# Kernel tuning notes

Measured on AMD Instinct MI355X. Metric: run time of the kernel, lower is better.

## Reference

```python
import jax, jax.numpy as jnp
import numpy as np

H = W = 2048
TANH_C = 1.1486328125  # probability-correction constant from the model
DEG2RAD = np.float32(np.pi / 180.0)

# Fire-spread direction angle (degrees, East=0, counterclockwise) from the
# neighbor at 3x3 window position (r, c) toward the center cell.
DIR_DEG = jnp.array([[315., 270., 225.],
                     [  0.,   0., 180.],
                     [ 45.,  90., 135.]], dtype=jnp.float32)
CENTER_MASK = jnp.ones((3, 3), jnp.float32).at[1, 1].set(0.0)  # exclude self


def _neighborhood(x):
    """x: [H,W] -> [H,W,3,3] with [i,j,r,c] = x[i+r-1, j+c-1], zero padded."""
    xp = jnp.pad(x, 1)
    return jnp.stack(
        [jnp.stack([xp[r:r + H, c:c + W] for c in range(3)], axis=-1)
         for r in range(3)], axis=-2)


def setup_inputs() -> dict:
    key = jax.random.key(0)
    ks = jax.random.split(key, 8)
    p_veg = jax.random.uniform(ks[0], (H, W), jnp.float32)
    p_den = jax.random.uniform(ks[1], (H, W), jnp.float32)
    wind_velocity = jax.random.uniform(ks[2], (H, W), jnp.float32) * 10.0
    wind_towards_direction = jax.random.uniform(ks[3], (H, W), jnp.float32) * 360.0
    slope = (jax.random.uniform(ks[4], (H, W, 3, 3), jnp.float32) - 0.5) * 60.0
    burning = jax.random.uniform(ks[5], (H, W)) < 0.01  # sparse initial ignition
    burned = jnp.zeros((H, W), dtype=bool)
    rand_ignite = jax.random.uniform(ks[6], (H, W), jnp.float32)
    rand_continue = jax.random.uniform(ks[7], (H, W), jnp.float32)
    return dict(
        p_veg=p_veg, p_den=p_den,
        wind_velocity=wind_velocity, wind_towards_direction=wind_towards_direction,
        slope=slope,
        a=jnp.float32(0.1), p_h=jnp.float32(0.3),
        c_1=jnp.float32(0.1), c_2=jnp.float32(0.1), p_continue=jnp.float32(0.3),
        rand_ignite=rand_ignite, rand_continue=rand_continue,
        burning=burning, burned=burned,
    )


def reference(p_veg, p_den, wind_velocity, wind_towards_direction, slope,
              a, p_h, c_1, c_2, p_continue,
              rand_ignite, rand_continue, burning, burned):
    # p_w = exp(c1*V) * exp(c2*V*(cos(theta_w)-1)), theta_w = angle between
    # wind direction and per-neighbor spread direction. [H,W,3,3]
    theta_w = (wind_towards_direction[..., None, None] - DIR_DEG) * DEG2RAD
    p_w = (jnp.exp(c_1 * wind_velocity)[..., None, None]
           * jnp.exp(c_2 * wind_velocity[..., None, None] * (jnp.cos(theta_w) - 1.0)))
    # p_s = exp(a * theta_s), slope angle in radians. [H,W,3,3]
    p_s = jnp.exp(a * slope * DEG2RAD)
    # p_propagate = tanh(c * p_h*(1+p_veg)*(1+p_den)*p_w*p_s)
    p_base = p_h * (1.0 + p_veg) * (1.0 + p_den)  # [H,W]
    p_prop = jnp.tanh(TANH_C * (p_base[..., None, None] * p_w * p_s))
    # 8-neighbor burning indicators (center masked out). [H,W,3,3]
    nbr_burning = _neighborhood(burning.astype(jnp.float32)) * CENTER_MASK
    # p_ignite = 1 - prod_j (1 - p_propagate_j * burning_j)
    p_ignite = 1.0 - jnp.prod(1.0 - p_prop * nbr_burning, axis=(-2, -1))
    # Stochastic state transition.
    burnable = ~burning & ~burned
    new_ignited = burnable & (rand_ignite < p_ignite)
    keep = burning & (rand_continue < p_continue)
    new_burning = new_ignited | keep
    new_burned = burned | (burning & ~keep)
    return p_ignite, jnp.stack([new_burning, new_burned])
```

## Files before the change

### kernel.cpp

```cpp
#include <hip/hip_runtime.h>
#include <math.h>

namespace {

constexpr int H = 2048;
constexpr int W = 2048;
constexpr float TANH_C  = 1.1486328125f;
constexpr float DEG2RAD = 0.017453292519943295f;

__global__ __launch_bounds__(256) void wildfire_step(
    const float* __restrict__ p_veg,  const float* __restrict__ p_den,
    const float* __restrict__ wind_v, const float* __restrict__ wind_d,
    const float* __restrict__ slope,
    const float* __restrict__ s_a,  const float* __restrict__ s_ph,
    const float* __restrict__ s_c1, const float* __restrict__ s_c2,
    const float* __restrict__ s_pc,
    const float* __restrict__ rand_ig, const float* __restrict__ rand_co,
    const int* __restrict__ burning, const int* __restrict__ burned,
    float* __restrict__ out)
{
    __shared__ float sb[3][260];
    const int t  = (int)threadIdx.x;
    const int i  = (int)blockIdx.y;
    const int j0 = (int)blockIdx.x * 256;
    const int j  = j0 + t;

    for (int r = 0; r < 3; ++r) {
        const int ii = i + r - 1;
        for (int c = t; c < 258; c += 256) {
            const int jj = j0 - 1 + c;
            float v = 0.f;
            if (ii >= 0 && ii < H && jj >= 0 && jj < W)
                v = burning[ii * W + jj] ? 1.f : 0.f;
            sb[r][c] = v;
        }
    }
    __syncthreads();

    const float b0 = sb[0][t], b1 = sb[0][t+1], b2 = sb[0][t+2];
    const float b3 = sb[1][t], bc = sb[1][t+1], b5 = sb[1][t+2];
    const float b6 = sb[2][t], b7 = sb[2][t+1], b8 = sb[2][t+2];

    const int   idx       = i * W + j;
    const bool  is_burning = (bc != 0.f);
    const int   was_burned = burned[idx];
    const float rco        = rand_co[idx];
    const float p_cont     = s_pc[0];

    const float any_n = b0 + b1 + b2 + b3 + b5 + b6 + b7 + b8;

    float p_ignite   = 0.f;
    bool  new_ignited = false;

    if (__any(any_n != 0.f)) {
        const float a   = s_a[0];
        const float p_h = s_ph[0];
        const float c1  = s_c1[0];
        const float c2  = s_c2[0];
        const float pv  = p_veg[idx];
        const float pd  = p_den[idx];
        const float wv  = wind_v[idx];
        const float wd  = wind_d[idx];

        const float ew     = expf(c1 * wv);
        const float cvw    = c2 * wv;
        const float p_base = (p_h * (1.f + pv)) * (1.f + pd);
        const float* sl    = slope + (size_t)idx * 9;

        float prod = 1.f;
#define NEIGHBOR(bk, dirdeg, si)                                           \
        if (__any(bk != 0.f)) {                                            \
            const float ct = cosf((wd - dirdeg) * DEG2RAD);                \
            const float pw = ew * expf(cvw * (ct - 1.f));                  \
            const float ps = expf((a * sl[si]) * DEG2RAD);                 \
            const float pp = tanhf(TANH_C * ((p_base * pw) * ps));         \
            prod *= 1.f - pp * bk;                                         \
        }
        NEIGHBOR(b0, 315.f, 0)
        NEIGHBOR(b1, 270.f, 1)
        NEIGHBOR(b2, 225.f, 2)
        NEIGHBOR(b3,   0.f, 3)
        NEIGHBOR(b5, 180.f, 5)
        NEIGHBOR(b6,  45.f, 6)
        NEIGHBOR(b7,  90.f, 7)
        NEIGHBOR(b8, 135.f, 8)
#undef NEIGHBOR
        p_ignite = 1.f - prod;

        const float rig = rand_ig[idx];
        new_ignited = (!is_burning) && (was_burned == 0) && (rig < p_ignite);
    }

    const bool keep = is_burning && (rco < p_cont);
    const bool nb   = new_ignited || keep;
    const bool nd   = (was_burned != 0) || (is_burning && !keep);

    out[idx]             = p_ignite;
    out[H * W + idx]     = nb ? 1.f : 0.f;
    out[2 * H * W + idx] = nd ? 1.f : 0.f;
}

}

extern "C" void kernel_launch(void* const* d_in, const int* in_sizes, int n_in,
                              void* d_out, int out_size, void* d_ws, size_t ws_size,
                              hipStream_t stream)
{
    (void)in_sizes; (void)n_in; (void)out_size; (void)d_ws; (void)ws_size;
    dim3 grid(W / 256, H, 1);
    dim3 block(256, 1, 1);
    hipLaunchKernelGGL(wildfire_step, grid, block, 0, stream,
        (const float*)d_in[0],  (const float*)d_in[1],
        (const float*)d_in[2],  (const float*)d_in[3],
        (const float*)d_in[4],
        (const float*)d_in[5],  (const float*)d_in[6],
        (const float*)d_in[7],  (const float*)d_in[8],
        (const float*)d_in[9],
        (const float*)d_in[10], (const float*)d_in[11],
        (const int*)d_in[12],   (const int*)d_in[13],
        (float*)d_out);
}
```

Measured before the change: 341.2 us.

## Replace per-neighbor trig and tanh with angle-addition and single-division product

Computes cos and sin of the wind angle once and derives each neighbor's cosine by the angle-addition identity with constant direction components. Each neighbor's two exps are folded into one exp(u) scaled by a precomputed factor. The term 1 - tanh(z) is rewritten as 2/(exp(2z)+1), so the product over neighbors becomes one division of accumulated numerators by denominators. All eight neighbors are now computed without per-neighbor wave-uniform branches, and all loads are issued up front. This cuts transcendental work and divergent branching but computes the unused neighbors too, and exp(2z) can overflow to inf for large z (that case still gives p_ignite near 1).

```diff
diff --git a/kernel.cpp b/kernel.cpp
--- a/kernel.cpp
+++ b/kernel.cpp
@@ -7,6 +7,7 @@
 constexpr int W = 2048;
 constexpr float TANH_C  = 1.1486328125f;
 constexpr float DEG2RAD = 0.017453292519943295f;
+constexpr float RT2H    = 0.70710678118654752f;
 
 __global__ __launch_bounds__(256) void wildfire_step(
     const float* __restrict__ p_veg,  const float* __restrict__ p_den,
@@ -41,7 +42,7 @@
     const float b3 = sb[1][t], bc = sb[1][t+1], b5 = sb[1][t+2];
     const float b6 = sb[2][t], b7 = sb[2][t+1], b8 = sb[2][t+2];
 
-    const int   idx       = i * W + j;
+    const int   idx        = i * W + j;
     const bool  is_burning = (bc != 0.f);
     const int   was_burned = burned[idx];
     const float rco        = rand_co[idx];
@@ -49,45 +50,53 @@
 
     const float any_n = b0 + b1 + b2 + b3 + b5 + b6 + b7 + b8;
 
-    float p_ignite   = 0.f;
+    float p_ignite    = 0.f;
     bool  new_ignited = false;
 
     if (__any(any_n != 0.f)) {
+        const float pv  = p_veg[idx];
+        const float pd  = p_den[idx];
+        const float wv  = wind_v[idx];
+        const float wd  = wind_d[idx];
+        const float rig = rand_ig[idx];
+        float sl[9];
+        __builtin_memcpy(sl, slope + (size_t)idx * 9, 9 * sizeof(float));
+
         const float a   = s_a[0];
         const float p_h = s_ph[0];
         const float c1  = s_c1[0];
         const float c2  = s_c2[0];
-        const float pv  = p_veg[idx];
-        const float pd  = p_den[idx];
-        const float wv  = wind_v[idx];
-        const float wd  = wind_d[idx];
 
-        const float ew     = expf(c1 * wv);
-        const float cvw    = c2 * wv;
+        const float wr  = wd * DEG2RAD;
+        const float cw  = cosf(wr);
+        const float sw  = sinf(wr);
+        const float ew  = expf(c1 * wv);
+        const float cvw = c2 * wv;
+        const float asl = a * DEG2RAD;
         const float p_base = (p_h * (1.f + pv)) * (1.f + pd);
-        const float* sl    = slope + (size_t)idx * 9;
+        const float Cz  = TANH_C * (p_base * ew);
 
-        float prod = 1.f;
-#define NEIGHBOR(bk, dirdeg, si)                                           \
-        if (__any(bk != 0.f)) {                                            \
-            const float ct = cosf((wd - dirdeg) * DEG2RAD);                \
-            const float pw = ew * expf(cvw * (ct - 1.f));                  \
-            const float ps = expf((a * sl[si]) * DEG2RAD);                 \
-            const float pp = tanhf(TANH_C * ((p_base * pw) * ps));         \
-            prod *= 1.f - pp * bk;                                         \
-        }
-        NEIGHBOR(b0, 315.f, 0)
-        NEIGHBOR(b1, 270.f, 1)
-        NEIGHBOR(b2, 225.f, 2)
-        NEIGHBOR(b3,   0.f, 3)
-        NEIGHBOR(b5, 180.f, 5)
-        NEIGHBOR(b6,  45.f, 6)
-        NEIGHBOR(b7,  90.f, 7)
-        NEIGHBOR(b8, 135.f, 8)
+#define NEIGHBOR(K, b, CK, SK, si)                                          \
+        const float ct##K = fmaf(cw, (CK), sw * (SK));                      \
+        const float u##K  = fmaf(cvw, ct##K - 1.f, asl * sl[si]);           \
+        const float z##K  = Cz * expf(u##K);                                \
+        const float E##K  = expf(z##K + z##K);                              \
+        const float d##K  = ((b) != 0.f) ? (E##K + 1.f) : 1.f;              \
+        const float n##K  = ((b) != 0.f) ? 2.f : 1.f;
+
+        NEIGHBOR(0, b0,  RT2H, -RT2H, 0)
+        NEIGHBOR(1, b1,  0.f,  -1.f,  1)
+        NEIGHBOR(2, b2, -RT2H, -RT2H, 2)
+        NEIGHBOR(3, b3,  1.f,   0.f,  3)
+        NEIGHBOR(5, b5, -1.f,   0.f,  5)
+        NEIGHBOR(6, b6,  RT2H,  RT2H, 6)
+        NEIGHBOR(7, b7,  0.f,   1.f,  7)
+        NEIGHBOR(8, b8, -RT2H,  RT2H, 8)
 #undef NEIGHBOR
-        p_ignite = 1.f - prod;
+        const float den = ((d0 * d1) * (d2 * d3)) * ((d5 * d6) * (d7 * d8));
+        const float num = ((n0 * n1) * (n2 * n3)) * ((n5 * n6) * (n7 * n8));
+        p_ignite = 1.f - num / den;
 
-        const float rig = rand_ig[idx];
         new_ignited = (!is_burning) && (was_burned == 0) && (rig < p_ignite);
     }
 
```

Result: faster. 326.9 us (-4.2%).
